# Kernel tuning notes

Hardware: AMD Instinct MI355X
Metric: run time of the kernel (lower is better)

## Reference

```python
import jax, jax.numpy as jnp
import numpy as np

VIEW_R = 32
SCALING = 16.0 / 8.0  # lora_alpha / r


def setup_inputs() -> dict:
    key = jax.random.key(0)
    ks = jax.random.split(key, 12)
    bs, S, d, r = 64, 256, 768, 8
    n = d // VIEW_R  # 24
    return {
        "x": jax.random.normal(ks[0], (bs, S, d), jnp.float32),
        "user_h": jax.random.normal(ks[1], (bs, d), jnp.float32),
        "item_h": jax.random.normal(ks[2], (bs, d), jnp.float32),
        "W": jax.random.normal(ks[3], (d, d), jnp.float32) * 0.02,   # base weight (out,in)
        "b": jax.random.normal(ks[4], (d,), jnp.float32) * 0.02,
        "A": jax.random.normal(ks[5], (r, d), jnp.float32) * 0.02,   # lora_A
        "B": jax.random.normal(ks[6], (d, r), jnp.float32) * 0.02,   # lora_B (zeros at init; randomized to exercise math)
        "Wu": jax.random.normal(ks[7], (d, d), jnp.float32) * 0.02,  # lora_U weight (out,in)
        "VU": jax.random.normal(ks[8], (n, VIEW_R), jnp.float32) * 0.02,
        "Wi": jax.random.normal(ks[9], (d, d), jnp.float32) * 0.02,  # lora_I weight
        "VI": jax.random.normal(ks[10], (n, VIEW_R), jnp.float32) * 0.02,
    }


def _kron_branch(x, h, Wlin, V):
    # original: weight[b, q*n_in + n, l*32 + m] = (h @ Wlin.T)[b, q, l] * V[n, m]
    #           result[b,s,:] = x[b,s,:] @ weight[b]
    # factorized form (same math, no (bs, d, d) intermediate):
    bs, S, d = x.shape
    n, m = V.shape
    q = VIEW_R
    l = d // VIEW_R
    wq = (h @ Wlin.T).reshape(bs, q, l)          # (b, q, l)
    x4 = x.reshape(bs, S, q, n)                  # d split as (q, n)
    t = jnp.einsum("bsqn,nm->bsqm", x4, V)
    out = jnp.einsum("bsqm,bql->bslm", t, wq)    # out index = l*32 + m
    return out.reshape(bs, S, d)


def reference(x, user_h, item_h, W, b, A, B, Wu, VU, Wi, VI):
    # F.linear + LoRA
    out = jnp.einsum("bsd,od->bso", x, W) + b
    out = out + jnp.einsum("bsd,rd,or->bso", x, A, B) * SCALING
    # user Kronecker low-rank per-sample weight branch
    out = out + _kron_branch(x, user_h, Wu, VU)
    # item branch
    out = out + _kron_branch(x, item_h, Wi, VI)
    return out
```

## Files before the change

### kernel.cpp

```cpp
#include <hip/hip_runtime.h>
#include <hip/hip_bf16.h>

typedef __bf16 bf16x8 __attribute__((ext_vector_type(8)));
typedef float f32x4 __attribute__((ext_vector_type(4)));
typedef unsigned short u16x8 __attribute__((ext_vector_type(8)));

__device__ __forceinline__ unsigned short f2bf(float f) {
    unsigned int u = __builtin_bit_cast(unsigned int, f);
    unsigned int r = (u + 0x7FFFu + ((u >> 16) & 1u)) >> 16;
    return (unsigned short)r;
}

__device__ __forceinline__ void load_lds_16(const void* g, void* lds) {
    __builtin_amdgcn_global_load_lds(
        (const __attribute__((address_space(1))) unsigned int*)g,
        (__attribute__((address_space(3))) unsigned int*)lds, 16, 0, 0);
}

__global__ void prep_kernel(const float* __restrict__ x, unsigned short* __restrict__ xb,
                            const float* __restrict__ W, const float* __restrict__ A,
                            const float* __restrict__ B, unsigned short* __restrict__ weffB,
                            const float* __restrict__ uh, const float* __restrict__ ih,
                            const float* __restrict__ Wu, const float* __restrict__ Wi,
                            float* __restrict__ wqu, float* __restrict__ wqi) {
    int bx = blockIdx.x;
    int t = threadIdx.x;
    if (bx < 6144) {
        int i = bx * 256 + t;
        const float4* xp = (const float4*)x;
        float4 a = xp[i * 2];
        float4 c = xp[i * 2 + 1];
        u16x8 r;
        r[0] = f2bf(a.x); r[1] = f2bf(a.y); r[2] = f2bf(a.z); r[3] = f2bf(a.w);
        r[4] = f2bf(c.x); r[5] = f2bf(c.y); r[6] = f2bf(c.z); r[7] = f2bf(c.w);
        *(u16x8*)(xb + (size_t)i * 8) = r;
    } else if (bx < 8448) {
        int idx = bx - 6144;
        int o = idx / 3;
        int k = (idx % 3) * 256 + t;
        float acc = W[o * 768 + k];
#pragma unroll
        for (int r = 0; r < 8; ++r) acc += 2.0f * B[o * 8 + r] * A[r * 768 + k];
        weffB[o * 768 + k] = f2bf(acc);
    } else {
        int b2 = bx - 8448;
        int og = b2 % 192;
        int rest = b2 / 192;
        int b = rest & 63;
        int br = rest >> 6;
        int wave = t >> 6, lane = t & 63;
        int o = og * 4 + wave;
        const float* h = (br ? ih : uh) + b * 768;
        const float* Wrow = (br ? Wi : Wu) + (size_t)o * 768;
        const float4* hp = (const float4*)(h + lane * 12);
        const float4* wp = (const float4*)(Wrow + lane * 12);
        float s = 0.0f;
#pragma unroll
        for (int j = 0; j < 3; ++j) {
            float4 hv = hp[j], wv = wp[j];
            s += hv.x * wv.x + hv.y * wv.y + hv.z * wv.z + hv.w * wv.w;
        }
#pragma unroll
        for (int off = 32; off; off >>= 1) s += __shfl_down(s, off);
        if (lane == 0) (br ? wqi : wqu)[b * 768 + o] = s;
    }
}

__global__ __launch_bounds__(256, 3) void gemm_fused_kernel(
    const unsigned short* __restrict__ Xb, const unsigned short* __restrict__ WeffB,
    const float* __restrict__ VU, const float* __restrict__ VI,
    const float* __restrict__ wqu, const float* __restrict__ wqi,
    const float* __restrict__ bias, float* __restrict__ out) {
    __shared__ __align__(16) unsigned short As[128 * 64];
    __shared__ __align__(16) unsigned short Bs[128 * 64];
    __shared__ __align__(16) unsigned int vui[32 * 26];
    __shared__ __align__(16) float wqs[32 * 8];
    __shared__ float bias_s[128];
    const int tid = threadIdx.x;
    const int wave = tid >> 6, lane = tid & 63;
    const int id = blockIdx.x;
    const int nt = id >> 7, rem = id & 127, b = rem >> 1, mt = rem & 1;
    const int s0 = mt * 128, n0 = nt * 128;

    for (int i = tid; i < 768; i += 256) {
        int n = i >> 5, m = i & 31;
        vui[m * 26 + n] = ((unsigned int)f2bf(VU[i]) << 16) | (unsigned int)f2bf(VI[i]);
    }
    {
        int q = tid >> 3, g = (tid >> 1) & 3, br = tid & 1;
        const float* wq = br ? wqi : wqu;
        wqs[tid] = wq[b * 768 + q * 24 + nt * 4 + g];
    }
    if (tid < 128) bias_s[tid] = bias[n0 + tid];
    __syncthreads();

    const unsigned short* Abase = Xb + (size_t)(b * 256 + s0) * 768;
    const unsigned short* Bbase = WeffB + (size_t)n0 * 768;
    const int wm = wave & 1, wn = wave >> 1;
    const int lrow = lane >> 3, lcp = lane & 7;
    const int rg = tid >> 3, cc = tid & 7;
    const int sl = cc ^ (rg & 7);
    const unsigned short* Wp0 = Bbase + (size_t)rg * 768 + cc * 8;

    f32x4 acc[4][4] = {};
    u16x8 wreg[4];
#pragma unroll
    for (int g = 0; g < 4; ++g) wreg[g] = *(const u16x8*)(Wp0 + (size_t)g * 32 * 768);

    for (int kk = 0; kk < 768; kk += 64) {
#pragma unroll
        for (int u = 0; u < 4; ++u) {
            int tA = wave * 4 + u;
            int r = tA * 8 + lrow;
            int c = lcp ^ (r & 7);
            load_lds_16(Abase + (size_t)r * 768 + kk + c * 8, (void*)(As + tA * 512));
        }
        {
            int kb = kk + cc * 8;
            int q = (kb * 2731) >> 16;
            int n0c = kb - q * 24;
            const unsigned int* vp = &vui[rg * 26 + n0c];
            uint2 pv01 = *(const uint2*)(vp);
            uint2 pv23 = *(const uint2*)(vp + 2);
            uint2 pv45 = *(const uint2*)(vp + 4);
            uint2 pv67 = *(const uint2*)(vp + 6);
            unsigned int pv[8] = {pv01.x, pv01.y, pv23.x, pv23.y, pv45.x, pv45.y, pv67.x, pv67.y};
            float fu[8], fi[8];
#pragma unroll
            for (int j = 0; j < 8; ++j) {
                fu[j] = __builtin_bit_cast(float, pv[j] & 0xFFFF0000u);
                fi[j] = __builtin_bit_cast(float, pv[j] << 16);
            }
            const float4* wp4 = (const float4*)&wqs[q * 8];
            float4 wa = wp4[0], wb = wp4[1];
            float wu[4] = {wa.x, wa.z, wb.x, wb.z};
            float wi[4] = {wa.y, wa.w, wb.y, wb.w};
#pragma unroll
            for (int g = 0; g < 4; ++g) {
                u16x8 kv;
#pragma unroll
                for (int j = 0; j < 8; ++j) {
                    float wf = __builtin_bit_cast(float, (unsigned int)wreg[g][j] << 16);
                    float v = wf + fu[j] * wu[g];
                    v = v + fi[j] * wi[g];
                    kv[j] = (unsigned short)(__builtin_bit_cast(unsigned int, v) >> 16);
                }
                *(u16x8*)(Bs + (g * 32 + rg) * 64 + sl * 8) = kv;
            }
        }
        if (kk < 704) {
            const unsigned short* Wn = Wp0 + kk + 64;
#pragma unroll
            for (int g = 0; g < 4; ++g) wreg[g] = *(const u16x8*)(Wn + (size_t)g * 32 * 768);
        }
        __syncthreads();
#pragma unroll
        for (int h = 0; h < 2; ++h) {
            const int cb = h * 4 + (lane >> 4);
            const int rl = lane & 15;
            bf16x8 af[4], bw[4];
#pragma unroll
            for (int i = 0; i < 4; ++i) {
                int r = wm * 64 + i * 16 + rl;
                int c = cb ^ (r & 7);
                af[i] = *(const bf16x8*)(As + r * 64 + c * 8);
            }
#pragma unroll
            for (int j = 0; j < 4; ++j) {
                int r = wn * 64 + j * 16 + rl;
                int c = cb ^ (r & 7);
                bw[j] = *(const bf16x8*)(Bs + r * 64 + c * 8);
            }
#pragma unroll
            for (int i = 0; i < 4; ++i)
#pragma unroll
                for (int j = 0; j < 4; ++j)
                    acc[i][j] = __builtin_amdgcn_mfma_f32_16x16x32_bf16(af[i], bw[j], acc[i][j], 0, 0, 0);
        }
        __syncthreads();
    }

    const int cl = lane & 15, rq = lane >> 4;
#pragma unroll
    for (int j = 0; j < 4; ++j) {
        int nn = wn * 64 + j * 16 + cl;
        float bv = bias_s[nn];
#pragma unroll
        for (int i = 0; i < 4; ++i) {
            int mrow = s0 + wm * 64 + i * 16 + rq * 4;
            float* op = out + (size_t)(b * 256 + mrow) * 768 + n0 + nn;
#pragma unroll
            for (int g = 0; g < 4; ++g) op[(size_t)g * 768] = acc[i][j][g] + bv;
        }
    }
}

__global__ void weff_kernel(const float* __restrict__ W, const float* __restrict__ A,
                            const float* __restrict__ B, float* __restrict__ Weff) {
    int o = blockIdx.x / 3;
    int k = (blockIdx.x % 3) * 256 + threadIdx.x;
    float acc = W[o * 768 + k];
#pragma unroll
    for (int r = 0; r < 8; ++r) acc += 2.0f * B[o * 8 + r] * A[r * 768 + k];
    Weff[o * 768 + k] = acc;
}

__global__ void wq2_kernel(const float* __restrict__ uh, const float* __restrict__ ih,
                           const float* __restrict__ Wu, const float* __restrict__ Wi,
                           float* __restrict__ wqu, float* __restrict__ wqi) {
    int bx = blockIdx.x;
    int og = bx % 192;
    int rest = bx / 192;
    int b = rest & 63;
    int br = rest >> 6;
    int wave = threadIdx.x >> 6, lane = threadIdx.x & 63;
    int o = og * 4 + wave;
    const float* h = (br ? ih : uh) + b * 768;
    const float* Wrow = (br ? Wi : Wu) + (size_t)o * 768;
    const float4* hp = (const float4*)(h + lane * 12);
    const float4* wp = (const float4*)(Wrow + lane * 12);
    float s = 0.0f;
#pragma unroll
    for (int j = 0; j < 3; ++j) {
        float4 hv = hp[j], wv = wp[j];
        s += hv.x * wv.x + hv.y * wv.y + hv.z * wv.z + hv.w * wv.w;
    }
#pragma unroll
    for (int off = 32; off; off >>= 1) s += __shfl_down(s, off);
    if (lane == 0) (br ? wqi : wqu)[b * 768 + o] = s;
}

__global__ void naive_kernel(const float* __restrict__ x, const float* __restrict__ Weff,
                             const float* __restrict__ wqu, const float* __restrict__ wqi,
                             const float* __restrict__ VU, const float* __restrict__ VI,
                             const float* __restrict__ bias, float* __restrict__ out) {
    int bs_ = blockIdx.x / 3;
    int chunk = blockIdx.x % 3;
    int b = bs_ >> 8;
    __shared__ float xs[768];
    for (int i = threadIdx.x; i < 768; i += 256) xs[i] = x[(size_t)bs_ * 768 + i];
    __syncthreads();
    int o = chunk * 256 + threadIdx.x;
    int m = o & 31, l = o >> 5;
    float acc = bias[o];
    for (int q = 0; q < 32; ++q) {
        float wu = wqu[b * 768 + q * 24 + l];
        float wi = wqi[b * 768 + q * 24 + l];
#pragma unroll
        for (int n = 0; n < 24; ++n) {
            int k = q * 24 + n;
            float w = Weff[o * 768 + k] + VU[n * 32 + m] * wu + VI[n * 32 + m] * wi;
            acc += xs[k] * w;
        }
    }
    out[(size_t)bs_ * 768 + o] = acc;
}

extern "C" void kernel_launch(void* const* d_in, const int* in_sizes, int n_in,
                              void* d_out, int out_size, void* d_ws, size_t ws_size,
                              hipStream_t stream) {
    const float* x  = (const float*)d_in[0];
    const float* uh = (const float*)d_in[1];
    const float* ih = (const float*)d_in[2];
    const float* W  = (const float*)d_in[3];
    const float* bv = (const float*)d_in[4];
    const float* A  = (const float*)d_in[5];
    const float* B  = (const float*)d_in[6];
    const float* Wu = (const float*)d_in[7];
    const float* VU = (const float*)d_in[8];
    const float* Wi = (const float*)d_in[9];
    const float* VI = (const float*)d_in[10];
    float* out = (float*)d_out;

    const size_t off_xb   = 0;
    const size_t off_weff = 25165824;
    const size_t off_wqu  = off_weff + 1179648;
    const size_t off_wqi  = off_wqu + 196608;
    const size_t need     = off_wqi + 196608;

    char* ws = (char*)d_ws;
    if (ws_size >= need) {
        unsigned short* xb    = (unsigned short*)(ws + off_xb);
        unsigned short* weffB = (unsigned short*)(ws + off_weff);
        float* wqu = (float*)(ws + off_wqu);
        float* wqi = (float*)(ws + off_wqi);
        prep_kernel<<<33024, 256, 0, stream>>>(x, xb, W, A, B, weffB, uh, ih, Wu, Wi, wqu, wqi);
        gemm_fused_kernel<<<768, 256, 0, stream>>>(xb, weffB, VU, VI, wqu, wqi, bv, out);
    } else {
        float* weff = (float*)ws;
        float* wqu  = weff + 589824;
        float* wqi  = wqu + 49152;
        weff_kernel<<<2304, 256, 0, stream>>>(W, A, B, weff);
        wq2_kernel<<<24576, 256, 0, stream>>>(uh, ih, Wu, Wi, wqu, wqi);
        naive_kernel<<<49152, 256, 0, stream>>>(x, weff, wqu, wqi, VU, VI, bv, out);
    }
}
```

Measured before the change: 160.5 us.

## Tile the wq projection through LDS and batch the x bf16 conversion

Replaces the per-output, wave-per-dot-product computation of h@Wlin.T (24576 blocks, each rereading W rows) with a 96-block LDS-tiled GEMM that reuses each W tile across 16 batch rows. The x-to-bf16 conversion now processes four chunks per thread with all loads issued first, so it needs fewer blocks. The wq blocks are scheduled first. Together these cut the prep grid from 33024 to 3936 blocks and reduce redundant global reads of Wu/Wi. The risk is that the 96 long-running tiled blocks become a serial tail inside the prep kernel.

```diff
diff --git a/kernel.cpp b/kernel.cpp
--- a/kernel.cpp
+++ b/kernel.cpp
@@ -17,25 +17,58 @@
         (__attribute__((address_space(3))) unsigned int*)lds, 16, 0, 0);
 }
 
-__global__ void prep_kernel(const float* __restrict__ x, unsigned short* __restrict__ xb,
-                            const float* __restrict__ W, const float* __restrict__ A,
-                            const float* __restrict__ B, unsigned short* __restrict__ weffB,
-                            const float* __restrict__ uh, const float* __restrict__ ih,
-                            const float* __restrict__ Wu, const float* __restrict__ Wi,
-                            float* __restrict__ wqu, float* __restrict__ wqi) {
-    int bx = blockIdx.x;
-    int t = threadIdx.x;
-    if (bx < 6144) {
-        int i = bx * 256 + t;
-        const float4* xp = (const float4*)x;
-        float4 a = xp[i * 2];
-        float4 c = xp[i * 2 + 1];
-        u16x8 r;
-        r[0] = f2bf(a.x); r[1] = f2bf(a.y); r[2] = f2bf(a.z); r[3] = f2bf(a.w);
-        r[4] = f2bf(c.x); r[5] = f2bf(c.y); r[6] = f2bf(c.z); r[7] = f2bf(c.w);
-        *(u16x8*)(xb + (size_t)i * 8) = r;
-    } else if (bx < 8448) {
-        int idx = bx - 6144;
+__global__ __launch_bounds__(256) void prep_kernel(
+    const float* __restrict__ x, unsigned short* __restrict__ xb,
+    const float* __restrict__ W, const float* __restrict__ A,
+    const float* __restrict__ B, unsigned short* __restrict__ weffB,
+    const float* __restrict__ uh, const float* __restrict__ ih,
+    const float* __restrict__ Wu, const float* __restrict__ Wi,
+    float* __restrict__ wqu, float* __restrict__ wqi) {
+    __shared__ float Wl[64 * 68];
+    __shared__ float Hl[16 * 68];
+    const int bx = blockIdx.x;
+    const int t = threadIdx.x;
+    if (bx < 96) {
+        const int br = bx / 48, rem = bx % 48;
+        const int ot = rem >> 2, bt = rem & 3;
+        const int o0 = ot * 64, b0 = bt * 16;
+        const float* h = (br ? ih : uh);
+        const float* Wm = (br ? Wi : Wu);
+        const int so = t >> 2, sq = (t & 3) * 16;
+        const int hr = t >> 4, hc = (t & 15) * 4;
+        const int b_l = t >> 4, o4 = (t & 15) * 4;
+        float acc0 = 0.f, acc1 = 0.f, acc2 = 0.f, acc3 = 0.f;
+        for (int kk = 0; kk < 768; kk += 64) {
+            const float* wrow = Wm + (o0 + so) * 768 + kk + sq;
+            float4 w0 = ((const float4*)wrow)[0];
+            float4 w1 = ((const float4*)wrow)[1];
+            float4 w2 = ((const float4*)wrow)[2];
+            float4 w3 = ((const float4*)wrow)[3];
+            float4 hv = *(const float4*)(h + (b0 + hr) * 768 + kk + hc);
+            Wl[(sq + 0) * 68 + so] = w0.x;  Wl[(sq + 1) * 68 + so] = w0.y;
+            Wl[(sq + 2) * 68 + so] = w0.z;  Wl[(sq + 3) * 68 + so] = w0.w;
+            Wl[(sq + 4) * 68 + so] = w1.x;  Wl[(sq + 5) * 68 + so] = w1.y;
+            Wl[(sq + 6) * 68 + so] = w1.z;  Wl[(sq + 7) * 68 + so] = w1.w;
+            Wl[(sq + 8) * 68 + so] = w2.x;  Wl[(sq + 9) * 68 + so] = w2.y;
+            Wl[(sq + 10) * 68 + so] = w2.z; Wl[(sq + 11) * 68 + so] = w2.w;
+            Wl[(sq + 12) * 68 + so] = w3.x; Wl[(sq + 13) * 68 + so] = w3.y;
+            Wl[(sq + 14) * 68 + so] = w3.z; Wl[(sq + 15) * 68 + so] = w3.w;
+            *(float4*)&Hl[hr * 68 + hc] = hv;
+            __syncthreads();
+#pragma unroll 8
+            for (int k = 0; k < 64; ++k) {
+                float hs = Hl[b_l * 68 + k];
+                float4 wv = *(const float4*)&Wl[k * 68 + o4];
+                acc0 += hs * wv.x; acc1 += hs * wv.y;
+                acc2 += hs * wv.z; acc3 += hs * wv.w;
+            }
+            __syncthreads();
+        }
+        float* wq = (br ? wqi : wqu);
+        float4 r; r.x = acc0; r.y = acc1; r.z = acc2; r.w = acc3;
+        *(float4*)&wq[(b0 + b_l) * 768 + o0 + o4] = r;
+    } else if (bx < 2400) {
+        int idx = bx - 96;
         int o = idx / 3;
         int k = (idx % 3) * 256 + t;
         float acc = W[o * 768 + k];
@@ -43,26 +76,24 @@
         for (int r = 0; r < 8; ++r) acc += 2.0f * B[o * 8 + r] * A[r * 768 + k];
         weffB[o * 768 + k] = f2bf(acc);
     } else {
-        int b2 = bx - 8448;
-        int og = b2 % 192;
-        int rest = b2 / 192;
-        int b = rest & 63;
-        int br = rest >> 6;
-        int wave = t >> 6, lane = t & 63;
-        int o = og * 4 + wave;
-        const float* h = (br ? ih : uh) + b * 768;
-        const float* Wrow = (br ? Wi : Wu) + (size_t)o * 768;
-        const float4* hp = (const float4*)(h + lane * 12);
-        const float4* wp = (const float4*)(Wrow + lane * 12);
-        float s = 0.0f;
-#pragma unroll
-        for (int j = 0; j < 3; ++j) {
-            float4 hv = hp[j], wv = wp[j];
-            s += hv.x * wv.x + hv.y * wv.y + hv.z * wv.z + hv.w * wv.w;
-        }
-#pragma unroll
-        for (int off = 32; off; off >>= 1) s += __shfl_down(s, off);
-        if (lane == 0) (br ? wqi : wqu)[b * 768 + o] = s;
+        int b2 = bx - 2400;
+        const float4* xp = (const float4*)x;
+        float4 a[4], c[4];
+        int i0 = b2 * 1024 + t;
+#pragma unroll
+        for (int u = 0; u < 4; ++u) {
+            int i = i0 + u * 256;
+            a[u] = xp[i * 2];
+            c[u] = xp[i * 2 + 1];
+        }
+#pragma unroll
+        for (int u = 0; u < 4; ++u) {
+            int i = i0 + u * 256;
+            u16x8 r;
+            r[0] = f2bf(a[u].x); r[1] = f2bf(a[u].y); r[2] = f2bf(a[u].z); r[3] = f2bf(a[u].w);
+            r[4] = f2bf(c[u].x); r[5] = f2bf(c[u].y); r[6] = f2bf(c[u].z); r[7] = f2bf(c[u].w);
+            *(u16x8*)(xb + (size_t)i * 8) = r;
+        }
     }
 }
 
@@ -284,7 +315,7 @@
         unsigned short* weffB = (unsigned short*)(ws + off_weff);
         float* wqu = (float*)(ws + off_wqu);
         float* wqi = (float*)(ws + off_wqi);
-        prep_kernel<<<33024, 256, 0, stream>>>(x, xb, W, A, B, weffB, uh, ih, Wu, Wi, wqu, wqi);
+        prep_kernel<<<3936, 256, 0, stream>>>(x, xb, W, A, B, weffB, uh, ih, Wu, Wi, wqu, wqi);
         gemm_fused_kernel<<<768, 256, 0, stream>>>(xb, weffB, VU, VI, wqu, wqi, bv, out);
     } else {
         float* weff = (float*)ws;
```

New measurement: 160.0 us. About the same (-0.3%).
